# Optimization experiments

Hardware: AMD Instinct MI355X
Metric: run time of the kernel (lower is better)

The kernel has to match this reference:

```python
import jax, jax.numpy as jnp
import numpy as np

N_HEAD = 16

def setup_inputs() -> dict:
    key = jax.random.key(0)
    k0, k1, k2, k3, k4 = jax.random.split(key, 5)
    B, T, C = 4, 2048, 1024
    x = jax.random.normal(k0, (B, T, C), dtype=jnp.float32)
    # torch nn.Linear weights are (out_features, in_features); scale like kaiming-uniform-ish
    s = 1.0 / np.sqrt(C)
    Wk = jax.random.uniform(k1, (C, C), jnp.float32, -s, s)
    Wq = jax.random.uniform(k2, (C, C), jnp.float32, -s, s)
    Wv = jax.random.uniform(k3, (C, C), jnp.float32, -s, s)
    Wo = jax.random.uniform(k4, (C, C), jnp.float32, -s, s)
    return {"x": x, "Wk": Wk, "Wq": Wq, "Wv": Wv, "Wo": Wo}

def reference(x, Wk, Wq, Wv, Wo):
    B, T, C = x.shape
    hs = C // N_HEAD
    # projections (torch Linear: y = x @ W.T), split heads -> (B, nh, T, hs)
    def proj(W):
        return (x @ W.T).reshape(B, T, N_HEAD, hs).transpose(0, 2, 1, 3)
    k = proj(Wk)
    q = proj(Wq)
    v = proj(Wv)
    # dot attention: scale by sqrt(head_dim) (k.shape[2] after transpose in source)
    score = jnp.einsum('bhqd,bhkd->bhqk', q, k) / jnp.sqrt(jnp.asarray(hs, x.dtype))
    # NOTE: source calls score.masked_fill(mask, -inf) without assignment -> mask has no effect.
    e = jax.nn.softmax(score, axis=-1)
    o = jnp.einsum('bhqk,bhkd->bhqd', e, v)          # (B, nh, T, hs)
    o = o.transpose(0, 2, 1, 3).reshape(B, T, C)     # merge heads
    o = o @ Wo.T                                      # final projection
    # dropout is identity in eval mode
    return o
```

## Files before the change

kernel.cpp:

```cpp
#include <hip/hip_runtime.h>
#include <hip/hip_bf16.h>
#include <cstddef>
#include <cstdint>

#define B_DIM 4
#define T_DIM 2048
#define C_DIM 1024
#define NHEAD 16
#define HS    64
#define QKV_LD 3072

typedef __attribute__((ext_vector_type(8))) short short8;
typedef __attribute__((ext_vector_type(4))) float f32x4;

__device__ __forceinline__ short f2bf(float x) {
    __hip_bfloat16 b = __float2bfloat16(x);
    return *reinterpret_cast<short*>(&b);
}

__device__ __forceinline__ void load_lds16(const void* g, void* l) {
    __builtin_amdgcn_global_load_lds(
        (const __attribute__((address_space(1))) void*)(g),
        (__attribute__((address_space(3))) void*)(l),
        16, 0, 0);
}

__global__ __launch_bounds__(256) void cast_bf16(
    const float* __restrict__ in, short* __restrict__ out, int n8)
{
    int i = blockIdx.x * 256 + threadIdx.x;
    if (i >= n8) return;
    const float4* p = (const float4*)in + (size_t)i * 2;
    float4 a = p[0], b = p[1];
    short8 o;
    o[0]=f2bf(a.x); o[1]=f2bf(a.y); o[2]=f2bf(a.z); o[3]=f2bf(a.w);
    o[4]=f2bf(b.x); o[5]=f2bf(b.y); o[6]=f2bf(b.z); o[7]=f2bf(b.w);
    *((short8*)out + i) = o;
}

#define BM 128
#define BN 128
#define BK 32

template<bool OUT_BF16>
__global__ __launch_bounds__(256) void gemm_bt_mfma(
    const short* __restrict__ A,
    const short* __restrict__ Bm,
    void* __restrict__ Cm,
    int M, int N, int K, float scale)
{
    __shared__ __align__(16) short smem[8192];
    short* As = smem;
    short* Bs = smem + 4096;

    const int m0 = blockIdx.y * BM;
    const int n0 = blockIdx.x * BN;
    const int t    = threadIdx.x;
    const int w    = t >> 6;
    const int lane = t & 63;
    const int l16  = lane & 15;
    const int quad = lane >> 4;
    const int wm   = w >> 1;
    const int wn   = w & 1;

    const int mS0 = t >> 2;
    const int qS  = (t & 3) ^ ((t >> 3) & 3);
    const short* aG0 = A  + (size_t)(m0 + mS0)      * K + qS * 8;
    const short* aG1 = A  + (size_t)(m0 + mS0 + 64) * K + qS * 8;
    const short* bG0 = Bm + (size_t)(n0 + mS0)      * K + qS * 8;
    const short* bG1 = Bm + (size_t)(n0 + mS0 + 64) * K + qS * 8;
    short* aL0 = As + (size_t)(w * 64) * 8;
    short* aL1 = As + (size_t)(256 + w * 64) * 8;
    short* bL0 = Bs + (size_t)(w * 64) * 8;
    short* bL1 = Bs + (size_t)(256 + w * 64) * 8;

    int a_off[4], b_off[4];
    #pragma unroll
    for (int i = 0; i < 4; ++i) {
        int am = wm * 64 + i * 16 + l16;
        a_off[i] = (am * 4 + (quad ^ ((am >> 1) & 3))) * 8;
        int bn = wn * 64 + i * 16 + l16;
        b_off[i] = (bn * 4 + (quad ^ ((bn >> 1) & 3))) * 8;
    }

    f32x4 acc[4][4];
    const f32x4 zero4 = {0.f, 0.f, 0.f, 0.f};
    #pragma unroll
    for (int i = 0; i < 4; ++i)
        #pragma unroll
        for (int j = 0; j < 4; ++j) acc[i][j] = zero4;

    for (int k0 = 0; k0 < K; k0 += BK) {
        __syncthreads();
        load_lds16(aG0 + k0, aL0);
        load_lds16(aG1 + k0, aL1);
        load_lds16(bG0 + k0, bL0);
        load_lds16(bG1 + k0, bL1);
        __syncthreads();

        short8 af[4], bf[4];
        #pragma unroll
        for (int i = 0; i < 4; ++i) {
            af[i] = *(const short8*)(As + a_off[i]);
            bf[i] = *(const short8*)(Bs + b_off[i]);
        }
        #pragma unroll
        for (int i = 0; i < 4; ++i)
            #pragma unroll
            for (int j = 0; j < 4; ++j)
                acc[i][j] = __builtin_amdgcn_mfma_f32_16x16x32_bf16(
                    af[i], bf[j], acc[i][j], 0, 0, 0);
    }

    #pragma unroll
    for (int i = 0; i < 4; ++i) {
        const int row_base = m0 + wm * 64 + i * 16 + quad * 4;
        #pragma unroll
        for (int j = 0; j < 4; ++j) {
            const int col = n0 + wn * 64 + j * 16 + l16;
            #pragma unroll
            for (int r = 0; r < 4; ++r) {
                const size_t idx = (size_t)(row_base + r) * N + col;
                if (OUT_BF16) ((short*)Cm)[idx] = f2bf(acc[i][j][r] * scale);
                else          ((float*)Cm)[idx] = acc[i][j][r] * scale;
            }
        }
    }
}

__global__ __launch_bounds__(256) void transpose_v(
    const short* __restrict__ Vb,
    short* __restrict__ Vt, int srcLD)
{
    const int t0 = blockIdx.x * 64;
    const int head = blockIdx.y;
    const int b = head >> 4, h = head & 15;

    __shared__ short Ls[64][72];

    const int t = threadIdx.x;
    const int r = t >> 2;
    const int c = (t & 3) * 16;

    const short* src = Vb + ((size_t)(b * T_DIM) + t0 + r) * srcLD + h * HS + c;
    *(short8*)&Ls[r][c]     = *(const short8*)src;
    *(short8*)&Ls[r][c + 8] = *(const short8*)(src + 8);
    __syncthreads();

    short tmp[16];
    #pragma unroll
    for (int i = 0; i < 16; ++i) tmp[i] = Ls[c + i][r];
    short* dst = Vt + ((size_t)head * HS + r) * T_DIM + t0 + c;
    *(short8*)dst       = *(short8*)&tmp[0];
    *(short8*)(dst + 8) = *(short8*)&tmp[8];
}

#define QSUB 4

__global__ __launch_bounds__(256, 2) void attn_mfma3(
    const short* __restrict__ Qb,
    const short* __restrict__ Kb,
    const short* __restrict__ Vt,
    short* __restrict__ O)
{
    const int i0   = blockIdx.x * (64 * QSUB);
    const int head = blockIdx.y;
    const int b = head >> 4, h = head & 15;

    const int t    = threadIdx.x;
    const int w    = t >> 6;
    const int lane = t & 63;
    const int l16  = lane & 15;
    const int quad = lane >> 4;

    __shared__ short Ks[64][72];
    __shared__ short Vts[64][72];

    short8 qf[QSUB][2];
    #pragma unroll
    for (int sub = 0; sub < QSUB; ++sub) {
        const short* qrow = Qb
            + ((size_t)(b * T_DIM) + i0 + sub * 64 + w * 16 + l16) * QKV_LD + h * HS;
        qf[sub][0] = *(const short8*)(qrow + quad * 8);
        qf[sub][1] = *(const short8*)(qrow + 32 + quad * 8);
    }

    const f32x4 zero4 = {0.f, 0.f, 0.f, 0.f};
    f32x4 oacc[QSUB][4];
    #pragma unroll
    for (int sub = 0; sub < QSUB; ++sub)
        #pragma unroll
        for (int dg = 0; dg < 4; ++dg) oacc[sub][dg] = zero4;
    float l_part[QSUB];
    #pragma unroll
    for (int sub = 0; sub < QSUB; ++sub) l_part[sub] = 0.0f;

    const int sr = t >> 2;
    const int sc = (t & 3) * 16;
    const int krow = (sr & 32) | ((sr & 4) << 2) | ((sr & 24) >> 1) | (sr & 3);
    const short* kgbase = Kb + (size_t)(b * T_DIM) * QKV_LD + h * HS;
    const short* vgbase = Vt + ((size_t)head * HS + sr) * T_DIM;

    for (int j0 = 0; j0 < T_DIM; j0 += 64) {
        __syncthreads();
        {
            const short* kp = kgbase + (size_t)(j0 + sr) * QKV_LD + sc;
            *(short8*)&Ks[krow][sc]     = *(const short8*)kp;
            *(short8*)&Ks[krow][sc + 8] = *(const short8*)(kp + 8);
            const short* vp = vgbase + j0 + sc;
            *(short8*)&Vts[sr][sc]      = *(const short8*)vp;
            *(short8*)&Vts[sr][sc + 8]  = *(const short8*)(vp + 8);
        }
        __syncthreads();

        short8 ka[4][2], va[4][2];
        #pragma unroll
        for (int kt = 0; kt < 4; ++kt) {
            ka[kt][0] = *(const short8*)&Ks[kt * 16 + l16][quad * 8];
            ka[kt][1] = *(const short8*)&Ks[kt * 16 + l16][32 + quad * 8];
            va[kt][0] = *(const short8*)&Vts[kt * 16 + l16][quad * 8];
            va[kt][1] = *(const short8*)&Vts[kt * 16 + l16][32 + quad * 8];
        }

        #pragma unroll
        for (int sub = 0; sub < QSUB; ++sub) {
            f32x4 s[4];
            #pragma unroll
            for (int kt = 0; kt < 4; ++kt) {
                f32x4 acc = zero4;
                acc = __builtin_amdgcn_mfma_f32_16x16x32_bf16(ka[kt][0], qf[sub][0], acc, 0, 0, 0);
                acc = __builtin_amdgcn_mfma_f32_16x16x32_bf16(ka[kt][1], qf[sub][1], acc, 0, 0, 0);
                s[kt] = acc;
            }

            short8 pa[2];
            float lp = l_part[sub];
            #pragma unroll
            for (int hh = 0; hh < 2; ++hh) {
                #pragma unroll
                for (int c = 0; c < 2; ++c) {
                    f32x4 sv = s[2 * hh + c];
                    #pragma unroll
                    for (int r = 0; r < 4; ++r) {
                        float p = __expf(sv[r] * 0.125f);
                        lp += p;
                        pa[hh][c * 4 + r] = f2bf(p);
                    }
                }
            }
            l_part[sub] = lp;

            #pragma unroll
            for (int dg = 0; dg < 4; ++dg) {
                oacc[sub][dg] = __builtin_amdgcn_mfma_f32_16x16x32_bf16(pa[0], va[dg][0], oacc[sub][dg], 0, 0, 0);
                oacc[sub][dg] = __builtin_amdgcn_mfma_f32_16x16x32_bf16(pa[1], va[dg][1], oacc[sub][dg], 0, 0, 0);
            }
        }
    }

    #pragma unroll
    for (int sub = 0; sub < QSUB; ++sub) {
        float lp = l_part[sub];
        lp += __shfl_xor(lp, 16);
        lp += __shfl_xor(lp, 32);
        float linv[4];
        #pragma unroll
        for (int r = 0; r < 4; ++r)
            linv[r] = 1.0f / __shfl(lp, quad * 4 + r);

        #pragma unroll
        for (int r = 0; r < 4; ++r) {
            short* orow = O + ((size_t)(b * T_DIM) + i0 + sub * 64 + w * 16 + quad * 4 + r) * C_DIM + h * HS;
            #pragma unroll
            for (int dg = 0; dg < 4; ++dg)
                orow[dg * 16 + l16] = f2bf(oacc[sub][dg][r] * linv[r]);
        }
    }
}

extern "C" void kernel_launch(void* const* d_in, const int* in_sizes, int n_in,
                              void* d_out, int out_size, void* d_ws, size_t ws_size,
                              hipStream_t stream) {
    const float* x  = (const float*)d_in[0];
    const float* Wk = (const float*)d_in[1];
    const float* Wq = (const float*)d_in[2];
    const float* Wv = (const float*)d_in[3];
    const float* Wo = (const float*)d_in[4];
    float* out = (float*)d_out;

    const int M = B_DIM * T_DIM;
    const size_t NE = (size_t)M * C_DIM;
    const size_t NB = 2 * NE;
    const size_t WB = (size_t)2 * C_DIM * C_DIM;
    const size_t WE = (size_t)C_DIM * C_DIM;

    char* ws = (char*)d_ws;
    short* xb   = (short*)(ws);
    short* Ob   = xb;
    short* QKVb = (short*)(ws + NB);
    short* Vtb  = (short*)(ws + 4 * NB);
    short* W3b  = (short*)(ws + 5 * NB);
    short* Wob  = (short*)(ws + 5 * NB + 3 * WB);

    cast_bf16<<<(int)(NE / 8 / 256), 256, 0, stream>>>(x, xb, (int)(NE / 8));
    const int wn8 = (int)(WE / 8);
    cast_bf16<<<wn8 / 256, 256, 0, stream>>>(Wq, W3b,          wn8);
    cast_bf16<<<wn8 / 256, 256, 0, stream>>>(Wk, W3b + WE,     wn8);
    cast_bf16<<<wn8 / 256, 256, 0, stream>>>(Wv, W3b + 2 * WE, wn8);
    cast_bf16<<<wn8 / 256, 256, 0, stream>>>(Wo, Wob,          wn8);

    gemm_bt_mfma<true><<<dim3(QKV_LD / BN, M / BM), 256, 0, stream>>>(
        xb, W3b, QKVb, M, QKV_LD, C_DIM, 1.0f);

    transpose_v<<<dim3(T_DIM / 64, B_DIM * NHEAD), 256, 0, stream>>>(
        QKVb + 2 * C_DIM, Vtb, QKV_LD);

    attn_mfma3<<<dim3(T_DIM / (64 * QSUB), B_DIM * NHEAD), 256, 0, stream>>>(
        QKVb, QKVb + C_DIM, Vtb, Ob);

    gemm_bt_mfma<false><<<dim3(C_DIM / BN, M / BM), 256, 0, stream>>>(
        Ob, Wob, out, M, C_DIM, C_DIM, 1.0f);
}
```

Before: 290.3 us.

## Use 512-thread attention blocks with fewer Q subtiles and batch weight casts

Attention blocks grow from 4 to 8 waves, each holding 2 query subtiles instead of 4, so per-thread register pressure drops and occupancy can rise. K/V tile loads are spread over 512 threads, and the K/V fragments are loaded per half-tile to shorten register live ranges. The exp is rewritten as exp2f with a prescaled constant. The four weight-cast launches are merged into one 2D launch to cut launch overhead. Wider blocks add barrier cost per K tile.

```diff
diff --git a/kernel.cpp b/kernel.cpp
--- a/kernel.cpp
+++ b/kernel.cpp
@@ -30,6 +30,29 @@
 {
     int i = blockIdx.x * 256 + threadIdx.x;
     if (i >= n8) return;
+    const float4* p = (const float4*)in + (size_t)i * 2;
+    float4 a = p[0], b = p[1];
+    short8 o;
+    o[0]=f2bf(a.x); o[1]=f2bf(a.y); o[2]=f2bf(a.z); o[3]=f2bf(a.w);
+    o[4]=f2bf(b.x); o[5]=f2bf(b.y); o[6]=f2bf(b.z); o[7]=f2bf(b.w);
+    *((short8*)out + i) = o;
+}
+
+__global__ __launch_bounds__(256) void cast_w4(
+    const float* __restrict__ w0, const float* __restrict__ w1,
+    const float* __restrict__ w2, const float* __restrict__ w3,
+    short* __restrict__ o0, short* __restrict__ o1,
+    short* __restrict__ o2, short* __restrict__ o3, int n8)
+{
+    int i = blockIdx.x * 256 + threadIdx.x;
+    if (i >= n8) return;
+    const float* in; short* out;
+    switch (blockIdx.y) {
+        case 0: in = w0; out = o0; break;
+        case 1: in = w1; out = o1; break;
+        case 2: in = w2; out = o2; break;
+        default: in = w3; out = o3; break;
+    }
     const float4* p = (const float4*)in + (size_t)i * 2;
     float4 a = p[0], b = p[1];
     short8 o;
@@ -155,15 +178,13 @@
     *(short8*)(dst + 8) = *(short8*)&tmp[8];
 }
 
-#define QSUB 4
-
-__global__ __launch_bounds__(256, 2) void attn_mfma3(
+__global__ __launch_bounds__(512, 4) void attn_mfma4(
     const short* __restrict__ Qb,
     const short* __restrict__ Kb,
     const short* __restrict__ Vt,
     short* __restrict__ O)
 {
-    const int i0   = blockIdx.x * (64 * QSUB);
+    const int i0   = blockIdx.x * 256;
     const int head = blockIdx.y;
     const int b = head >> 4, h = head & 15;
 
@@ -176,90 +197,79 @@
     __shared__ short Ks[64][72];
     __shared__ short Vts[64][72];
 
-    short8 qf[QSUB][2];
-    #pragma unroll
-    for (int sub = 0; sub < QSUB; ++sub) {
+    short8 qf[2][2];
+    #pragma unroll
+    for (int sub = 0; sub < 2; ++sub) {
         const short* qrow = Qb
-            + ((size_t)(b * T_DIM) + i0 + sub * 64 + w * 16 + l16) * QKV_LD + h * HS;
+            + ((size_t)(b * T_DIM) + i0 + sub * 128 + w * 16 + l16) * QKV_LD + h * HS;
         qf[sub][0] = *(const short8*)(qrow + quad * 8);
         qf[sub][1] = *(const short8*)(qrow + 32 + quad * 8);
     }
 
     const f32x4 zero4 = {0.f, 0.f, 0.f, 0.f};
-    f32x4 oacc[QSUB][4];
-    #pragma unroll
-    for (int sub = 0; sub < QSUB; ++sub)
+    f32x4 oacc[2][4];
+    #pragma unroll
+    for (int sub = 0; sub < 2; ++sub)
         #pragma unroll
         for (int dg = 0; dg < 4; ++dg) oacc[sub][dg] = zero4;
-    float l_part[QSUB];
-    #pragma unroll
-    for (int sub = 0; sub < QSUB; ++sub) l_part[sub] = 0.0f;
-
-    const int sr = t >> 2;
-    const int sc = (t & 3) * 16;
+    float l_part[2] = {0.f, 0.f};
+
+    const int sr = t >> 3;
+    const int sc = (t & 7) * 8;
     const int krow = (sr & 32) | ((sr & 4) << 2) | ((sr & 24) >> 1) | (sr & 3);
     const short* kgbase = Kb + (size_t)(b * T_DIM) * QKV_LD + h * HS;
     const short* vgbase = Vt + ((size_t)head * HS + sr) * T_DIM;
 
     for (int j0 = 0; j0 < T_DIM; j0 += 64) {
         __syncthreads();
-        {
-            const short* kp = kgbase + (size_t)(j0 + sr) * QKV_LD + sc;
-            *(short8*)&Ks[krow][sc]     = *(const short8*)kp;
-            *(short8*)&Ks[krow][sc + 8] = *(const short8*)(kp + 8);
-            const short* vp = vgbase + j0 + sc;
-            *(short8*)&Vts[sr][sc]      = *(const short8*)vp;
-            *(short8*)&Vts[sr][sc + 8]  = *(const short8*)(vp + 8);
-        }
+        *(short8*)&Ks[krow][sc] = *(const short8*)(kgbase + (size_t)(j0 + sr) * QKV_LD + sc);
+        *(short8*)&Vts[sr][sc]  = *(const short8*)(vgbase + j0 + sc);
         __syncthreads();
 
-        short8 ka[4][2], va[4][2];
-        #pragma unroll
-        for (int kt = 0; kt < 4; ++kt) {
-            ka[kt][0] = *(const short8*)&Ks[kt * 16 + l16][quad * 8];
-            ka[kt][1] = *(const short8*)&Ks[kt * 16 + l16][32 + quad * 8];
-            va[kt][0] = *(const short8*)&Vts[kt * 16 + l16][quad * 8];
-            va[kt][1] = *(const short8*)&Vts[kt * 16 + l16][32 + quad * 8];
-        }
-
-        #pragma unroll
-        for (int sub = 0; sub < QSUB; ++sub) {
-            f32x4 s[4];
-            #pragma unroll
-            for (int kt = 0; kt < 4; ++kt) {
-                f32x4 acc = zero4;
-                acc = __builtin_amdgcn_mfma_f32_16x16x32_bf16(ka[kt][0], qf[sub][0], acc, 0, 0, 0);
-                acc = __builtin_amdgcn_mfma_f32_16x16x32_bf16(ka[kt][1], qf[sub][1], acc, 0, 0, 0);
-                s[kt] = acc;
+        #pragma unroll
+        for (int hh = 0; hh < 2; ++hh) {
+            short8 ka[2][2], va[4];
+            #pragma unroll
+            for (int c = 0; c < 2; ++c) {
+                const int kt = 2 * hh + c;
+                ka[c][0] = *(const short8*)&Ks[kt * 16 + l16][quad * 8];
+                ka[c][1] = *(const short8*)&Ks[kt * 16 + l16][32 + quad * 8];
             }
-
-            short8 pa[2];
-            float lp = l_part[sub];
-            #pragma unroll
-            for (int hh = 0; hh < 2; ++hh) {
+            #pragma unroll
+            for (int dg = 0; dg < 4; ++dg)
+                va[dg] = *(const short8*)&Vts[dg * 16 + l16][hh * 32 + quad * 8];
+
+            #pragma unroll
+            for (int sub = 0; sub < 2; ++sub) {
+                f32x4 s[2];
                 #pragma unroll
                 for (int c = 0; c < 2; ++c) {
-                    f32x4 sv = s[2 * hh + c];
+                    f32x4 acc = zero4;
+                    acc = __builtin_amdgcn_mfma_f32_16x16x32_bf16(ka[c][0], qf[sub][0], acc, 0, 0, 0);
+                    acc = __builtin_amdgcn_mfma_f32_16x16x32_bf16(ka[c][1], qf[sub][1], acc, 0, 0, 0);
+                    s[c] = acc;
+                }
+                short8 pa;
+                float lp = l_part[sub];
+                #pragma unroll
+                for (int c = 0; c < 2; ++c)
                     #pragma unroll
                     for (int r = 0; r < 4; ++r) {
-                        float p = __expf(sv[r] * 0.125f);
+                        float p = exp2f(s[c][r] * 0.1803368801f);
                         lp += p;
-                        pa[hh][c * 4 + r] = f2bf(p);
+                        pa[c * 4 + r] = f2bf(p);
                     }
-                }
-            }
-            l_part[sub] = lp;
-
-            #pragma unroll
-            for (int dg = 0; dg < 4; ++dg) {
-                oacc[sub][dg] = __builtin_amdgcn_mfma_f32_16x16x32_bf16(pa[0], va[dg][0], oacc[sub][dg], 0, 0, 0);
-                oacc[sub][dg] = __builtin_amdgcn_mfma_f32_16x16x32_bf16(pa[1], va[dg][1], oacc[sub][dg], 0, 0, 0);
+                l_part[sub] = lp;
+                #pragma unroll
+                for (int dg = 0; dg < 4; ++dg)
+                    oacc[sub][dg] = __builtin_amdgcn_mfma_f32_16x16x32_bf16(
+                        pa, va[dg], oacc[sub][dg], 0, 0, 0);
             }
         }
     }
 
     #pragma unroll
-    for (int sub = 0; sub < QSUB; ++sub) {
+    for (int sub = 0; sub < 2; ++sub) {
         float lp = l_part[sub];
         lp += __shfl_xor(lp, 16);
         lp += __shfl_xor(lp, 32);
@@ -270,7 +280,7 @@
 
         #pragma unroll
         for (int r = 0; r < 4; ++r) {
-            short* orow = O + ((size_t)(b * T_DIM) + i0 + sub * 64 + w * 16 + quad * 4 + r) * C_DIM + h * HS;
+            short* orow = O + ((size_t)(b * T_DIM) + i0 + sub * 128 + w * 16 + quad * 4 + r) * C_DIM + h * HS;
             #pragma unroll
             for (int dg = 0; dg < 4; ++dg)
                 orow[dg * 16 + l16] = f2bf(oacc[sub][dg][r] * linv[r]);
@@ -304,10 +314,8 @@
 
     cast_bf16<<<(int)(NE / 8 / 256), 256, 0, stream>>>(x, xb, (int)(NE / 8));
     const int wn8 = (int)(WE / 8);
-    cast_bf16<<<wn8 / 256, 256, 0, stream>>>(Wq, W3b,          wn8);
-    cast_bf16<<<wn8 / 256, 256, 0, stream>>>(Wk, W3b + WE,     wn8);
-    cast_bf16<<<wn8 / 256, 256, 0, stream>>>(Wv, W3b + 2 * WE, wn8);
-    cast_bf16<<<wn8 / 256, 256, 0, stream>>>(Wo, Wob,          wn8);
+    cast_w4<<<dim3(wn8 / 256, 4), 256, 0, stream>>>(
+        Wq, Wk, Wv, Wo, W3b, W3b + WE, W3b + 2 * WE, Wob, wn8);
 
     gemm_bt_mfma<true><<<dim3(QKV_LD / BN, M / BM), 256, 0, stream>>>(
         xb, W3b, QKVb, M, QKV_LD, C_DIM, 1.0f);
@@ -315,7 +323,7 @@
     transpose_v<<<dim3(T_DIM / 64, B_DIM * NHEAD), 256, 0, stream>>>(
         QKVb + 2 * C_DIM, Vtb, QKV_LD);
 
-    attn_mfma3<<<dim3(T_DIM / (64 * QSUB), B_DIM * NHEAD), 256, 0, stream>>>(
+    attn_mfma4<<<dim3(T_DIM / 256, B_DIM * NHEAD), 512, 0, stream>>>(
         QKVb, QKVb + C_DIM, Vtb, Ob);
 
     gemm_bt_mfma<false><<<dim3(C_DIM / BN, M / BM), 256, 0, stream>>>(
```

Measured after the change: 306.5 us. +5.6%, slower.

## Split attention over key halves, fuse V transpose into QKV GEMM epilogue

Applied to the files above, without the earlier changes.

Attention gains a z grid dimension that splits the key range in half. Each half writes unnormalized bf16 partial outputs and row sums, and a new combine kernel adds and normalizes them, which doubles the block count and raises the occupancy hint to 4. The QKV GEMM epilogue now writes Q (pre-scaled by log2e/8 so the softmax can use exp2), K, and transposed V directly, removing the separate transpose kernel. The five cast launches are merged into one. In exchange it adds a combine pass over the full output, extra workspace, and an extra bf16 rounding of the partial outputs.

```diff
diff --git a/kernel.cpp b/kernel.cpp
--- a/kernel.cpp
+++ b/kernel.cpp
@@ -2,20 +2,27 @@
 #include <hip/hip_bf16.h>
 #include <cstddef>
 #include <cstdint>
+#include <cstring>
 
 #define B_DIM 4
 #define T_DIM 2048
 #define C_DIM 1024
 #define NHEAD 16
 #define HS    64
-#define QKV_LD 3072
+
+#define QSCALE 0.1803368801111204f
 
 typedef __attribute__((ext_vector_type(8))) short short8;
+typedef __attribute__((ext_vector_type(4))) short short4v;
 typedef __attribute__((ext_vector_type(4))) float f32x4;
 
 __device__ __forceinline__ short f2bf(float x) {
     __hip_bfloat16 b = __float2bfloat16(x);
     return *reinterpret_cast<short*>(&b);
+}
+__device__ __forceinline__ float b2f(short s) {
+    unsigned u = ((unsigned)(unsigned short)s) << 16;
+    float f; __builtin_memcpy(&f, &u, 4); return f;
 }
 
 __device__ __forceinline__ void load_lds16(const void* g, void* l) {
@@ -25,10 +32,22 @@
         16, 0, 0);
 }
 
-__global__ __launch_bounds__(256) void cast_bf16(
-    const float* __restrict__ in, short* __restrict__ out, int n8)
+__global__ __launch_bounds__(256) void cast_all(
+    const float* __restrict__ x,
+    const float* __restrict__ Wq, const float* __restrict__ Wk,
+    const float* __restrict__ Wv, const float* __restrict__ Wo,
+    short* __restrict__ xb, short* __restrict__ W3b, short* __restrict__ Wob,
+    int xn8, int wn8)
 {
     int i = blockIdx.x * 256 + threadIdx.x;
+    const float* in; short* out; int n8;
+    switch (blockIdx.y) {
+        case 0:  in = x;  out = xb;             n8 = xn8; break;
+        case 1:  in = Wq; out = W3b;            n8 = wn8; break;
+        case 2:  in = Wk; out = W3b + (size_t)wn8 * 8;      n8 = wn8; break;
+        case 3:  in = Wv; out = W3b + (size_t)wn8 * 16;     n8 = wn8; break;
+        default: in = Wo; out = Wob;            n8 = wn8; break;
+    }
     if (i >= n8) return;
     const float4* p = (const float4*)in + (size_t)i * 2;
     float4 a = p[0], b = p[1];
@@ -42,12 +61,13 @@
 #define BN 128
 #define BK 32
 
-template<bool OUT_BF16>
+template<int MODE>
 __global__ __launch_bounds__(256) void gemm_bt_mfma(
     const short* __restrict__ A,
     const short* __restrict__ Bm,
-    void* __restrict__ Cm,
-    int M, int N, int K, float scale)
+    float* __restrict__ Cf,
+    short* __restrict__ Qp, short* __restrict__ Kp, short* __restrict__ Vtp,
+    int M, int N, int K, float qscale)
 {
     __shared__ __align__(16) short smem[8192];
     short* As = smem;
@@ -112,60 +132,72 @@
                     af[i], bf[j], acc[i][j], 0, 0, 0);
     }
 
-    #pragma unroll
-    for (int i = 0; i < 4; ++i) {
-        const int row_base = m0 + wm * 64 + i * 16 + quad * 4;
-        #pragma unroll
-        for (int j = 0; j < 4; ++j) {
-            const int col = n0 + wn * 64 + j * 16 + l16;
-            #pragma unroll
-            for (int r = 0; r < 4; ++r) {
-                const size_t idx = (size_t)(row_base + r) * N + col;
-                if (OUT_BF16) ((short*)Cm)[idx] = f2bf(acc[i][j][r] * scale);
-                else          ((float*)Cm)[idx] = acc[i][j][r] * scale;
-            }
-        }
-    }
-}
-
-__global__ __launch_bounds__(256) void transpose_v(
-    const short* __restrict__ Vb,
-    short* __restrict__ Vt, int srcLD)
-{
-    const int t0 = blockIdx.x * 64;
-    const int head = blockIdx.y;
-    const int b = head >> 4, h = head & 15;
-
-    __shared__ short Ls[64][72];
-
-    const int t = threadIdx.x;
-    const int r = t >> 2;
-    const int c = (t & 3) * 16;
-
-    const short* src = Vb + ((size_t)(b * T_DIM) + t0 + r) * srcLD + h * HS + c;
-    *(short8*)&Ls[r][c]     = *(const short8*)src;
-    *(short8*)&Ls[r][c + 8] = *(const short8*)(src + 8);
-    __syncthreads();
-
-    short tmp[16];
-    #pragma unroll
-    for (int i = 0; i < 16; ++i) tmp[i] = Ls[c + i][r];
-    short* dst = Vt + ((size_t)head * HS + r) * T_DIM + t0 + c;
-    *(short8*)dst       = *(short8*)&tmp[0];
-    *(short8*)(dst + 8) = *(short8*)&tmp[8];
+    if (MODE == 0) {
+        #pragma unroll
+        for (int i = 0; i < 4; ++i) {
+            const int row_base = m0 + wm * 64 + i * 16 + quad * 4;
+            #pragma unroll
+            for (int j = 0; j < 4; ++j) {
+                const int col = n0 + wn * 64 + j * 16 + l16;
+                #pragma unroll
+                for (int r = 0; r < 4; ++r)
+                    Cf[(size_t)(row_base + r) * N + col] = acc[i][j][r];
+            }
+        }
+    } else {
+        const int region = n0 >> 10;
+        if (region < 2) {
+            short* dst = (region == 0) ? Qp : Kp;
+            const float sc = (region == 0) ? qscale : 1.0f;
+            #pragma unroll
+            for (int i = 0; i < 4; ++i) {
+                const int row_base = m0 + wm * 64 + i * 16 + quad * 4;
+                #pragma unroll
+                for (int j = 0; j < 4; ++j) {
+                    const int colw = (n0 & 1023) + wn * 64 + j * 16 + l16;
+                    #pragma unroll
+                    for (int r = 0; r < 4; ++r)
+                        dst[(size_t)(row_base + r) * C_DIM + colw] =
+                            f2bf(acc[i][j][r] * sc);
+                }
+            }
+        } else {
+            #pragma unroll
+            for (int i = 0; i < 4; ++i) {
+                const int row_base = m0 + wm * 64 + i * 16 + quad * 4;
+                const int bI = row_base >> 11;
+                const int t0 = row_base & 2047;
+                #pragma unroll
+                for (int j = 0; j < 4; ++j) {
+                    const int d_full = (n0 - 2048) + wn * 64 + j * 16 + l16;
+                    const int head = d_full >> 6;
+                    const int d    = d_full & 63;
+                    short4v o;
+                    o.x = f2bf(acc[i][j][0]); o.y = f2bf(acc[i][j][1]);
+                    o.z = f2bf(acc[i][j][2]); o.w = f2bf(acc[i][j][3]);
+                    *(short4v*)(Vtp + ((size_t)((bI * NHEAD + head) * HS + d) << 11) + t0) = o;
+                }
+            }
+        }
+    }
 }
 
 #define QSUB 4
 
-__global__ __launch_bounds__(256, 2) void attn_mfma3(
+__global__ __launch_bounds__(256, 4) void attn_mfma5(
     const short* __restrict__ Qb,
     const short* __restrict__ Kb,
     const short* __restrict__ Vt,
-    short* __restrict__ O)
+    short* __restrict__ O0,
+    short* __restrict__ O1,
+    float* __restrict__ Lp)
 {
     const int i0   = blockIdx.x * (64 * QSUB);
     const int head = blockIdx.y;
+    const int z    = blockIdx.z;
     const int b = head >> 4, h = head & 15;
+
+    short* __restrict__ Op = z ? O1 : O0;
 
     const int t    = threadIdx.x;
     const int w    = t >> 6;
@@ -180,7 +212,7 @@
     #pragma unroll
     for (int sub = 0; sub < QSUB; ++sub) {
         const short* qrow = Qb
-            + ((size_t)(b * T_DIM) + i0 + sub * 64 + w * 16 + l16) * QKV_LD + h * HS;
+            + ((size_t)(b * T_DIM) + i0 + sub * 64 + w * 16 + l16) * C_DIM + h * HS;
         qf[sub][0] = *(const short8*)(qrow + quad * 8);
         qf[sub][1] = *(const short8*)(qrow + 32 + quad * 8);
     }
@@ -198,13 +230,14 @@
     const int sr = t >> 2;
     const int sc = (t & 3) * 16;
     const int krow = (sr & 32) | ((sr & 4) << 2) | ((sr & 24) >> 1) | (sr & 3);
-    const short* kgbase = Kb + (size_t)(b * T_DIM) * QKV_LD + h * HS;
+    const short* kgbase = Kb + (size_t)(b * T_DIM) * C_DIM + h * HS;
     const short* vgbase = Vt + ((size_t)head * HS + sr) * T_DIM;
 
-    for (int j0 = 0; j0 < T_DIM; j0 += 64) {
+    const int jbeg = z * (T_DIM / 2), jend = jbeg + T_DIM / 2;
+    for (int j0 = jbeg; j0 < jend; j0 += 64) {
         __syncthreads();
         {
-            const short* kp = kgbase + (size_t)(j0 + sr) * QKV_LD + sc;
+            const short* kp = kgbase + (size_t)(j0 + sr) * C_DIM + sc;
             *(short8*)&Ks[krow][sc]     = *(const short8*)kp;
             *(short8*)&Ks[krow][sc + 8] = *(const short8*)(kp + 8);
             const short* vp = vgbase + j0 + sc;
@@ -242,7 +275,7 @@
                     f32x4 sv = s[2 * hh + c];
                     #pragma unroll
                     for (int r = 0; r < 4; ++r) {
-                        float p = __expf(sv[r] * 0.125f);
+                        float p = exp2f(sv[r]);
                         lp += p;
                         pa[hh][c * 4 + r] = f2bf(p);
                     }
@@ -263,19 +296,41 @@
         float lp = l_part[sub];
         lp += __shfl_xor(lp, 16);
         lp += __shfl_xor(lp, 32);
-        float linv[4];
-        #pragma unroll
-        for (int r = 0; r < 4; ++r)
-            linv[r] = 1.0f / __shfl(lp, quad * 4 + r);
+        if (quad == 0)
+            Lp[((size_t)(z * B_DIM * NHEAD + head) << 11) + i0 + sub * 64 + w * 16 + l16] = lp;
 
         #pragma unroll
         for (int r = 0; r < 4; ++r) {
-            short* orow = O + ((size_t)(b * T_DIM) + i0 + sub * 64 + w * 16 + quad * 4 + r) * C_DIM + h * HS;
+            short* orow = Op + ((size_t)(b * T_DIM) + i0 + sub * 64 + w * 16 + quad * 4 + r) * C_DIM + h * HS;
             #pragma unroll
             for (int dg = 0; dg < 4; ++dg)
-                orow[dg * 16 + l16] = f2bf(oacc[sub][dg][r] * linv[r]);
-        }
-    }
+                orow[dg * 16 + l16] = f2bf(oacc[sub][dg][r]);
+        }
+    }
+}
+
+__global__ __launch_bounds__(256) void combine_o(
+    const short* __restrict__ O1,
+    const float* __restrict__ Lp,
+    short* __restrict__ O0_and_out, int n8)
+{
+    int i = blockIdx.x * 256 + threadIdx.x;
+    if (i >= n8) return;
+    const int row  = i >> 7;
+    const int cg   = i & 127;
+    const int bI   = row >> 11;
+    const int tI   = row & 2047;
+    const int head = cg >> 3;
+    const size_t lidx = ((size_t)(bI * NHEAD + head) << 11) + tI;
+    const float linv = 1.0f / (Lp[lidx] + Lp[lidx + ((size_t)B_DIM * NHEAD << 11)]);
+
+    short8 a = *((const short8*)O0_and_out + i);
+    short8 c = *((const short8*)O1 + i);
+    short8 o;
+    #pragma unroll
+    for (int e = 0; e < 8; ++e)
+        o[e] = f2bf((b2f(a[e]) + b2f(c[e])) * linv);
+    *((short8*)O0_and_out + i) = o;
 }
 
 extern "C" void kernel_launch(void* const* d_in, const int* in_sizes, int n_in,
@@ -295,29 +350,28 @@
     const size_t WE = (size_t)C_DIM * C_DIM;
 
     char* ws = (char*)d_ws;
-    short* xb   = (short*)(ws);
-    short* Ob   = xb;
-    short* QKVb = (short*)(ws + NB);
-    short* Vtb  = (short*)(ws + 4 * NB);
-    short* W3b  = (short*)(ws + 5 * NB);
-    short* Wob  = (short*)(ws + 5 * NB + 3 * WB);
-
-    cast_bf16<<<(int)(NE / 8 / 256), 256, 0, stream>>>(x, xb, (int)(NE / 8));
-    const int wn8 = (int)(WE / 8);
-    cast_bf16<<<wn8 / 256, 256, 0, stream>>>(Wq, W3b,          wn8);
-    cast_bf16<<<wn8 / 256, 256, 0, stream>>>(Wk, W3b + WE,     wn8);
-    cast_bf16<<<wn8 / 256, 256, 0, stream>>>(Wv, W3b + 2 * WE, wn8);
-    cast_bf16<<<wn8 / 256, 256, 0, stream>>>(Wo, Wob,          wn8);
-
-    gemm_bt_mfma<true><<<dim3(QKV_LD / BN, M / BM), 256, 0, stream>>>(
-        xb, W3b, QKVb, M, QKV_LD, C_DIM, 1.0f);
-
-    transpose_v<<<dim3(T_DIM / 64, B_DIM * NHEAD), 256, 0, stream>>>(
-        QKVb + 2 * C_DIM, Vtb, QKV_LD);
-
-    attn_mfma3<<<dim3(T_DIM / (64 * QSUB), B_DIM * NHEAD), 256, 0, stream>>>(
-        QKVb, QKVb + C_DIM, Vtb, Ob);
-
-    gemm_bt_mfma<false><<<dim3(C_DIM / BN, M / BM), 256, 0, stream>>>(
-        Ob, Wob, out, M, C_DIM, C_DIM, 1.0f);
-}
+    short* xb  = (short*)(ws);
+    short* Op1 = xb;
+    short* Qb  = (short*)(ws + 1 * NB);
+    short* Kb  = (short*)(ws + 2 * NB);
+    short* Vtb = (short*)(ws + 3 * NB);
+    short* W3b = (short*)(ws + 4 * NB);
+    short* Wob = (short*)(ws + 4 * NB + 3 * WB);
+    short* Op0 = (short*)(ws + 4 * NB + 4 * WB);
+    float* Lp  = (float*)(ws + 5 * NB + 4 * WB);
+
+    cast_all<<<dim3((int)(NE / 8 / 256), 5), 256, 0, stream>>>(
+        x, Wq, Wk, Wv, Wo, xb, W3b, Wob, (int)(NE / 8), (int)(WE / 8));
+
+    gemm_bt_mfma<2><<<dim3(3 * C_DIM / BN, M / BM), 256, 0, stream>>>(
+        xb, W3b, nullptr, Qb, Kb, Vtb, M, 3 * C_DIM, C_DIM, QSCALE);
+
+    attn_mfma5<<<dim3(T_DIM / (64 * QSUB), B_DIM * NHEAD, 2), 256, 0, stream>>>(
+        Qb, Kb, Vtb, Op0, Op1, Lp);
+
+    combine_o<<<(int)(NE / 8 / 256), 256, 0, stream>>>(
+        Op1, Lp, Op0, (int)(NE / 8));
+
+    gemm_bt_mfma<0><<<dim3(C_DIM / BN, M / BM), 256, 0, stream>>>(
+        Op0, Wob, out, nullptr, nullptr, nullptr, M, C_DIM, C_DIM, 1.0f);
+}
```

New measurement: 868.4 us. +199.1%, slower.
